# Optimization experiments

Hardware: AMD Instinct MI355X
Metric: run time of the kernel (lower is better)

The kernel has to match this reference:

```python
import jax, jax.numpy as jnp
import numpy as np

IN_CHANNELS = 2  # density + 1 value channel
OUT_CHANNELS = 64
INIT_LENGTH_SCALE = 0.03125


def setup_inputs() -> dict:
    key = jax.random.key(0)
    ks = jax.random.split(key, 5)
    B, N_IN, N_OUT = 8, 1024, 4096
    # locations in roughly [-2, 2]
    x = jax.random.uniform(ks[0], (B, N_IN, 2), jnp.float32, -2.0, 2.0)
    y = jax.random.normal(ks[1], (B, N_IN, 1), jnp.float32)
    t = jax.random.uniform(ks[2], (B, N_OUT, 2), jnp.float32, -2.0, 2.0)
    # learned params
    sigma = jnp.full((IN_CHANNELS,), np.log(INIT_LENGTH_SCALE), jnp.float32)
    W = jax.random.normal(ks[3], (OUT_CHANNELS, IN_CHANNELS), jnp.float32) / jnp.sqrt(IN_CHANNELS)
    b = jnp.zeros((OUT_CHANNELS,), jnp.float32)
    return {"x": x, "y": y, "t": t, "sigma": sigma, "W": W, "b": b}


def reference(x, y, t, sigma, W, b):
    # pairwise squared distances over 2D coords: (B, n_in, n_out)
    dists = ((x[:, :, None, 0] - t[:, None, :, 0]) ** 2
             + (x[:, :, None, 1] - t[:, None, :, 1]) ** 2)
    scales = jnp.exp(sigma)  # (C,) with C = in_channels = 2
    # RBF weights per channel: (B, n_in, n_out, C)
    wt = jnp.exp(-0.5 * dists[..., None] / scales ** 2)
    B, n_in, _ = x.shape
    density = jnp.ones((B, n_in, 1), x.dtype)
    dens_y = jnp.concatenate([density, y], axis=2)  # (B, n_in, C)
    # weighted sum over context points: (B, n_out, C)
    y_out = jnp.einsum('bnc,bnmc->bmc', dens_y, wt)
    dens, conv = y_out[..., :1], y_out[..., 1:]
    feat = jnp.concatenate([dens, conv / (dens + 1e-8)], axis=-1)  # (B, n_out, C)
    # pointwise linear to out_channels
    return jnp.einsum('bmc,oc->bmo', feat, W) + b
```

## Files before the change

### kernel.cpp

```cpp
#include <hip/hip_runtime.h>


#define N_IN  1024
#define N_OUT 4096
#define OUTC  64

__global__ __launch_bounds__(256) void convdeepset_kernel(
    const float* __restrict__ x,
    const float* __restrict__ y,
    const float* __restrict__ t,
    const float* __restrict__ sigma,
    const float* __restrict__ W,
    const float* __restrict__ bias,
    float* __restrict__ out)
{
    __shared__ float2 xs[N_IN];
    __shared__ float  ys[N_IN];
    __shared__ float  dens_part[4 * 64];
    __shared__ float  conv_part[4 * 64];
    __shared__ float  dens_tot[64];
    __shared__ float  conv_tot[64];

    const int tid = threadIdx.x;
    const int b   = blockIdx.x >> 6;
    const int m0  = (blockIdx.x & 63) << 6;

    const float2* xg = (const float2*)(x + (size_t)b * N_IN * 2);
    const float*  yg = y + (size_t)b * N_IN;
    for (int i = tid; i < N_IN; i += 256) {
        xs[i] = xg[i];
        ys[i] = yg[i];
    }

    const float log2e = 1.44269504088896340736f;
    const float k0 = -0.5f * __expf(-2.0f * sigma[0]) * log2e;
    const float k1 = -0.5f * __expf(-2.0f * sigma[1]) * log2e;

    __syncthreads();

    const int wave = tid >> 6;
    const int lane = tid & 63;
    const int m    = m0 + lane;
    const float2 tv = ((const float2*)(t + ((size_t)b * N_OUT + m) * 2))[0];

    float dens = 0.f, conv = 0.f;
    const int nbeg = wave * (N_IN / 4);
    #pragma unroll 4
    for (int n = nbeg; n < nbeg + N_IN / 4; ++n) {
        float2 xv = xs[n];
        float  yv = ys[n];
        float dx = xv.x - tv.x;
        float dy = xv.y - tv.y;
        float d  = dx * dx + dy * dy;
        dens += __builtin_amdgcn_exp2f(d * k0);
        conv += yv * __builtin_amdgcn_exp2f(d * k1);
    }
    dens_part[wave * 64 + lane] = dens;
    conv_part[wave * 64 + lane] = conv;
    __syncthreads();

    if (tid < 64) {
        float dt = dens_part[tid] + dens_part[64 + tid] +
                   dens_part[128 + tid] + dens_part[192 + tid];
        float ct = conv_part[tid] + conv_part[64 + tid] +
                   conv_part[128 + tid] + conv_part[192 + tid];
        dens_tot[tid] = dt;
        conv_tot[tid] = ct / (dt + 1e-8f);
    }
    __syncthreads();

    const int o = tid & 63;
    const int g = tid >> 6;
    const float w0 = W[o * 2 + 0];
    const float w1 = W[o * 2 + 1];
    const float bo = bias[o];
    float* outb = out + ((size_t)b * N_OUT + m0) * OUTC;
    #pragma unroll
    for (int i = 0; i < 16; ++i) {
        int mm = g * 16 + i;
        outb[mm * OUTC + o] = dens_tot[mm] * w0 + conv_tot[mm] * w1 + bo;
    }
}

extern "C" void kernel_launch(void* const* d_in, const int* in_sizes, int n_in,
                              void* d_out, int out_size, void* d_ws, size_t ws_size,
                              hipStream_t stream) {
    const float* x     = (const float*)d_in[0];
    const float* y     = (const float*)d_in[1];
    const float* t     = (const float*)d_in[2];
    const float* sigma = (const float*)d_in[3];
    const float* W     = (const float*)d_in[4];
    const float* bias  = (const float*)d_in[5];
    float* out = (float*)d_out;

    convdeepset_kernel<<<dim3(512), dim3(256), 0, stream>>>(
        x, y, t, sigma, W, bias, out);
}
```

Baseline: 79.73 us.

## Prescale coordinates, share one exp when length scales match, and enlarge blocks

Coordinates are pre-multiplied by sqrt of the exponent scale so each distance feeds exp2 directly. When both channel scales are equal, a single exp is reused for the density and value sums, halving transcendental work. Otherwise the second exponent is obtained by scaling the argument. Blocks grow to 1024 threads handling 128 outputs, with each thread computing two targets and 16 waves splitting the inputs. This adds a two-level reduction and gives only 256 blocks, which may underfill the GPU.

```diff
diff --git a/kernel.cpp b/kernel.cpp
--- a/kernel.cpp
+++ b/kernel.cpp
@@ -1,11 +1,10 @@
 #include <hip/hip_runtime.h>
 
 
-#define N_IN  1024
-#define N_OUT 4096
-#define OUTC  64
+#define OUTC 64
+#define MB   128
 
-__global__ __launch_bounds__(256) void convdeepset_kernel(
+__global__ __launch_bounds__(1024) void convdeepset_kernel(
     const float* __restrict__ x,
     const float* __restrict__ y,
     const float* __restrict__ t,
@@ -14,58 +13,124 @@
     const float* __restrict__ bias,
     float* __restrict__ out)
 {
-    __shared__ float2 xs[N_IN];
-    __shared__ float  ys[N_IN];
-    __shared__ float  dens_part[4 * 64];
-    __shared__ float  conv_part[4 * 64];
-    __shared__ float  dens_tot[64];
-    __shared__ float  conv_tot[64];
+    __shared__ float4 pk[512];
+    __shared__ float2 yy[512];
+    __shared__ float  dens_part[16*MB];
+    __shared__ float  conv_part[16*MB];
+    __shared__ float  sums[2*MB];
+    __shared__ float  dens_tot[MB];
+    __shared__ float  ratio[MB];
 
     const int tid = threadIdx.x;
-    const int b   = blockIdx.x >> 6;
-    const int m0  = (blockIdx.x & 63) << 6;
-
-    const float2* xg = (const float2*)(x + (size_t)b * N_IN * 2);
-    const float*  yg = y + (size_t)b * N_IN;
-    for (int i = tid; i < N_IN; i += 256) {
-        xs[i] = xg[i];
-        ys[i] = yg[i];
-    }
+    const int b   = blockIdx.x >> 5;
+    const int m0  = (blockIdx.x & 31) * MB;
 
     const float log2e = 1.44269504088896340736f;
     const float k0 = -0.5f * __expf(-2.0f * sigma[0]) * log2e;
     const float k1 = -0.5f * __expf(-2.0f * sigma[1]) * log2e;
+    const float s0 = sqrtf(-k0);
+    const float r  = k1 / k0;
+
+    if (tid < 512) {
+        const float4* xg = (const float4*)(x + (size_t)b * 2048);
+        float4 xv = xg[tid];
+        xv.x *= s0; xv.y *= s0; xv.z *= s0; xv.w *= s0;
+        pk[tid] = xv;
+    } else {
+        const float2* yg = (const float2*)(y + (size_t)b * 1024);
+        yy[tid - 512] = yg[tid - 512];
+    }
+
+    const int wave = tid >> 6;
+    const int lane = tid & 63;
+    const float2* tg = (const float2*)(t + ((size_t)b * 4096 + m0) * 2);
+    const float2 ta = tg[lane];
+    const float2 tb = tg[64 + lane];
+    const float t0x = ta.x * s0, t0y = ta.y * s0;
+    const float t1x = tb.x * s0, t1y = tb.y * s0;
 
     __syncthreads();
 
-    const int wave = tid >> 6;
-    const int lane = tid & 63;
-    const int m    = m0 + lane;
-    const float2 tv = ((const float2*)(t + ((size_t)b * N_OUT + m) * 2))[0];
+    float d0 = 0.f, c0 = 0.f, d1 = 0.f, c1 = 0.f;
+    const int ibeg = wave * 32;
 
-    float dens = 0.f, conv = 0.f;
-    const int nbeg = wave * (N_IN / 4);
-    #pragma unroll 4
-    for (int n = nbeg; n < nbeg + N_IN / 4; ++n) {
-        float2 xv = xs[n];
-        float  yv = ys[n];
-        float dx = xv.x - tv.x;
-        float dy = xv.y - tv.y;
-        float d  = dx * dx + dy * dy;
-        dens += __builtin_amdgcn_exp2f(d * k0);
-        conv += yv * __builtin_amdgcn_exp2f(d * k1);
+    if (r == 1.0f) {
+        #pragma unroll 4
+        for (int i = ibeg; i < ibeg + 32; ++i) {
+            const float4 p  = pk[i];
+            const float2 yv = yy[i];
+            {
+                float dx = p.x - t0x, dy = p.y - t0y;
+                float e = __builtin_amdgcn_exp2f(fmaf(dx, -dx, -(dy * dy)));
+                d0 += e; c0 = fmaf(yv.x, e, c0);
+            }
+            {
+                float dx = p.x - t1x, dy = p.y - t1y;
+                float e = __builtin_amdgcn_exp2f(fmaf(dx, -dx, -(dy * dy)));
+                d1 += e; c1 = fmaf(yv.x, e, c1);
+            }
+            {
+                float dx = p.z - t0x, dy = p.w - t0y;
+                float e = __builtin_amdgcn_exp2f(fmaf(dx, -dx, -(dy * dy)));
+                d0 += e; c0 = fmaf(yv.y, e, c0);
+            }
+            {
+                float dx = p.z - t1x, dy = p.w - t1y;
+                float e = __builtin_amdgcn_exp2f(fmaf(dx, -dx, -(dy * dy)));
+                d1 += e; c1 = fmaf(yv.y, e, c1);
+            }
+        }
+    } else {
+        #pragma unroll 2
+        for (int i = ibeg; i < ibeg + 32; ++i) {
+            const float4 p  = pk[i];
+            const float2 yv = yy[i];
+            {
+                float dx = p.x - t0x, dy = p.y - t0y;
+                float a  = fmaf(dx, -dx, -(dy * dy));
+                d0 += __builtin_amdgcn_exp2f(a);
+                c0 = fmaf(yv.x, __builtin_amdgcn_exp2f(a * r), c0);
+            }
+            {
+                float dx = p.x - t1x, dy = p.y - t1y;
+                float a  = fmaf(dx, -dx, -(dy * dy));
+                d1 += __builtin_amdgcn_exp2f(a);
+                c1 = fmaf(yv.x, __builtin_amdgcn_exp2f(a * r), c1);
+            }
+            {
+                float dx = p.z - t0x, dy = p.w - t0y;
+                float a  = fmaf(dx, -dx, -(dy * dy));
+                d0 += __builtin_amdgcn_exp2f(a);
+                c0 = fmaf(yv.y, __builtin_amdgcn_exp2f(a * r), c0);
+            }
+            {
+                float dx = p.z - t1x, dy = p.w - t1y;
+                float a  = fmaf(dx, -dx, -(dy * dy));
+                d1 += __builtin_amdgcn_exp2f(a);
+                c1 = fmaf(yv.y, __builtin_amdgcn_exp2f(a * r), c1);
+            }
+        }
     }
-    dens_part[wave * 64 + lane] = dens;
-    conv_part[wave * 64 + lane] = conv;
+
+    dens_part[wave * MB + lane]      = d0;
+    dens_part[wave * MB + 64 + lane] = d1;
+    conv_part[wave * MB + lane]      = c0;
+    conv_part[wave * MB + 64 + lane] = c1;
     __syncthreads();
 
-    if (tid < 64) {
-        float dt = dens_part[tid] + dens_part[64 + tid] +
-                   dens_part[128 + tid] + dens_part[192 + tid];
-        float ct = conv_part[tid] + conv_part[64 + tid] +
-                   conv_part[128 + tid] + conv_part[192 + tid];
+    if (tid < 256) {
+        const int m = tid & (MB - 1);
+        const float* src = (tid < MB) ? dens_part : conv_part;
+        float s = 0.f;
+        #pragma unroll
+        for (int w = 0; w < 16; ++w) s += src[w * MB + m];
+        sums[tid] = s;
+    }
+    __syncthreads();
+    if (tid < MB) {
+        float dt = sums[tid];
         dens_tot[tid] = dt;
-        conv_tot[tid] = ct / (dt + 1e-8f);
+        ratio[tid]    = sums[MB + tid] / (dt + 1e-8f);
     }
     __syncthreads();
 
@@ -74,11 +139,11 @@
     const float w0 = W[o * 2 + 0];
     const float w1 = W[o * 2 + 1];
     const float bo = bias[o];
-    float* outb = out + ((size_t)b * N_OUT + m0) * OUTC;
+    float* outb = out + ((size_t)b * 4096 + m0) * OUTC;
     #pragma unroll
-    for (int i = 0; i < 16; ++i) {
-        int mm = g * 16 + i;
-        outb[mm * OUTC + o] = dens_tot[mm] * w0 + conv_tot[mm] * w1 + bo;
+    for (int i = 0; i < 8; ++i) {
+        int mm = g * 8 + i;
+        outb[mm * OUTC + o] = fmaf(dens_tot[mm], w0, fmaf(ratio[mm], w1, bo));
     }
 }
 
@@ -93,6 +158,6 @@
     const float* bias  = (const float*)d_in[5];
     float* out = (float*)d_out;
 
-    convdeepset_kernel<<<dim3(512), dim3(256), 0, stream>>>(
+    convdeepset_kernel<<<dim3(256), dim3(1024), 0, stream>>>(
         x, y, t, sigma, W, bias, out);
 }
```

Result: faster. 74.28 us (-6.8%).

## Expand squared distance into dot-product form, share exp when scales match, widen blocks

Applied to the files above, without the earlier changes.

Pre-scales the context points into a packed (2x, 2y, -|x|^2, y) float4, so each pair's exponent becomes two FMAs plus an add instead of differences and squares. When both channel length scales are equal, one exp2 is shared between the density and conv sums; otherwise the second exponent is obtained by scaling the argument. Blocks grow to 1024 threads (16 waves) that split the context points, with a two-stage LDS reduction. The expanded-distance form can lose precision through cancellation, and the larger block raises reduction and synchronisation cost.

```diff
diff --git a/kernel.cpp b/kernel.cpp
--- a/kernel.cpp
+++ b/kernel.cpp
@@ -1,11 +1,11 @@
 #include <hip/hip_runtime.h>
 
 
-#define N_IN  1024
-#define N_OUT 4096
-#define OUTC  64
+#define OUTC 64
+#define MB   64
+#define NW   16
 
-__global__ __launch_bounds__(256) void convdeepset_kernel(
+__global__ __launch_bounds__(1024, 8) void convdeepset_kernel(
     const float* __restrict__ x,
     const float* __restrict__ y,
     const float* __restrict__ t,
@@ -14,58 +14,79 @@
     const float* __restrict__ bias,
     float* __restrict__ out)
 {
-    __shared__ float2 xs[N_IN];
-    __shared__ float  ys[N_IN];
-    __shared__ float  dens_part[4 * 64];
-    __shared__ float  conv_part[4 * 64];
-    __shared__ float  dens_tot[64];
-    __shared__ float  conv_tot[64];
+    __shared__ float4 pk[1024];
+    __shared__ float  dens_part[NW*MB];
+    __shared__ float  conv_part[NW*MB];
+    __shared__ float  sums[2*MB];
+    __shared__ float  dens_tot[MB];
+    __shared__ float  ratio[MB];
 
     const int tid = threadIdx.x;
     const int b   = blockIdx.x >> 6;
-    const int m0  = (blockIdx.x & 63) << 6;
-
-    const float2* xg = (const float2*)(x + (size_t)b * N_IN * 2);
-    const float*  yg = y + (size_t)b * N_IN;
-    for (int i = tid; i < N_IN; i += 256) {
-        xs[i] = xg[i];
-        ys[i] = yg[i];
-    }
+    const int m0  = (blockIdx.x & 63) * MB;
 
     const float log2e = 1.44269504088896340736f;
     const float k0 = -0.5f * __expf(-2.0f * sigma[0]) * log2e;
     const float k1 = -0.5f * __expf(-2.0f * sigma[1]) * log2e;
+    const float s0 = sqrtf(-k0);
+    const float r  = k1 / k0;
+
+    {
+        const float2 xv = ((const float2*)(x + (size_t)b * 2048))[tid];
+        const float  yv = y[(size_t)b * 1024 + tid];
+        const float sx = xv.x * s0, sy = xv.y * s0;
+        pk[tid] = make_float4(sx + sx, sy + sy,
+                              -fmaf(sx, sx, sy * sy), yv);
+    }
+
+    const int wave = tid >> 6;
+    const int lane = tid & 63;
+    const float2 tv = ((const float2*)(t + ((size_t)b * 4096 + m0) * 2))[lane];
+    const float u  = tv.x * s0;
+    const float v  = tv.y * s0;
+    const float cm = -fmaf(u, u, v * v);
 
     __syncthreads();
 
-    const int wave = tid >> 6;
-    const int lane = tid & 63;
-    const int m    = m0 + lane;
-    const float2 tv = ((const float2*)(t + ((size_t)b * N_OUT + m) * 2))[0];
+    float dacc = 0.f, cacc = 0.f;
+    const int ibeg = wave * 64;
 
-    float dens = 0.f, conv = 0.f;
-    const int nbeg = wave * (N_IN / 4);
-    #pragma unroll 4
-    for (int n = nbeg; n < nbeg + N_IN / 4; ++n) {
-        float2 xv = xs[n];
-        float  yv = ys[n];
-        float dx = xv.x - tv.x;
-        float dy = xv.y - tv.y;
-        float d  = dx * dx + dy * dy;
-        dens += __builtin_amdgcn_exp2f(d * k0);
-        conv += yv * __builtin_amdgcn_exp2f(d * k1);
+    if (r == 1.0f) {
+        #pragma unroll 4
+        for (int i = ibeg; i < ibeg + 64; ++i) {
+            const float4 p = pk[i];
+            float arg = fmaf(p.x, u, fmaf(p.y, v, p.z + cm));
+            float e   = __builtin_amdgcn_exp2f(arg);
+            dacc += e;
+            cacc = fmaf(p.w, e, cacc);
+        }
+    } else {
+        #pragma unroll 2
+        for (int i = ibeg; i < ibeg + 64; ++i) {
+            const float4 p = pk[i];
+            float arg = fmaf(p.x, u, fmaf(p.y, v, p.z + cm));
+            dacc += __builtin_amdgcn_exp2f(arg);
+            cacc = fmaf(p.w, __builtin_amdgcn_exp2f(arg * r), cacc);
+        }
     }
-    dens_part[wave * 64 + lane] = dens;
-    conv_part[wave * 64 + lane] = conv;
+
+    dens_part[wave * MB + lane] = dacc;
+    conv_part[wave * MB + lane] = cacc;
     __syncthreads();
 
-    if (tid < 64) {
-        float dt = dens_part[tid] + dens_part[64 + tid] +
-                   dens_part[128 + tid] + dens_part[192 + tid];
-        float ct = conv_part[tid] + conv_part[64 + tid] +
-                   conv_part[128 + tid] + conv_part[192 + tid];
+    if (tid < 2 * MB) {
+        const int m = tid & (MB - 1);
+        const float* src = (tid < MB) ? dens_part : conv_part;
+        float s = 0.f;
+        #pragma unroll
+        for (int w = 0; w < NW; ++w) s += src[w * MB + m];
+        sums[tid] = s;
+    }
+    __syncthreads();
+    if (tid < MB) {
+        float dt = sums[tid];
         dens_tot[tid] = dt;
-        conv_tot[tid] = ct / (dt + 1e-8f);
+        ratio[tid]    = sums[MB + tid] / (dt + 1e-8f);
     }
     __syncthreads();
 
@@ -74,11 +95,11 @@
     const float w0 = W[o * 2 + 0];
     const float w1 = W[o * 2 + 1];
     const float bo = bias[o];
-    float* outb = out + ((size_t)b * N_OUT + m0) * OUTC;
+    float* outb = out + ((size_t)b * 4096 + m0) * OUTC;
     #pragma unroll
-    for (int i = 0; i < 16; ++i) {
-        int mm = g * 16 + i;
-        outb[mm * OUTC + o] = dens_tot[mm] * w0 + conv_tot[mm] * w1 + bo;
+    for (int i = 0; i < 4; ++i) {
+        int mm = g * 4 + i;
+        outb[mm * OUTC + o] = fmaf(dens_tot[mm], w0, fmaf(ratio[mm], w1, bo));
     }
 }
 
@@ -93,6 +114,6 @@
     const float* bias  = (const float*)d_in[5];
     float* out = (float*)d_out;
 
-    convdeepset_kernel<<<dim3(512), dim3(256), 0, stream>>>(
+    convdeepset_kernel<<<dim3(512), dim3(1024), 0, stream>>>(
         x, y, t, sigma, W, bias, out);
 }
```

New measurement: 72.57 us. 9.0% less time.
